# Kernel tuning notes

Measured on AMD Instinct MI355X. Metric: run time of the kernel, lower is better.

Reference implementation:

```python
import math
import jax, jax.numpy as jnp
import numpy as np

N, C, T, V = 256, 128, 64, 25
OUT, H = 128, 4
D = OUT // H  # 32
MAX_LEN = 64
KSIZE = 9
EPS = 1e-5
NEG = -1e9


def setup_inputs() -> dict:
    key = jax.random.key(0)
    ks = jax.random.split(key, 20)
    std = 0.02
    return {
        "x": jax.random.normal(ks[0], (N, C, T, V), jnp.float32),
        # BatchNorm (eval mode) on input
        "bn_gamma": 1.0 + 0.1 * jax.random.normal(ks[1], (C,), jnp.float32),
        "bn_beta": 0.1 * jax.random.normal(ks[2], (C,), jnp.float32),
        "bn_mean": 0.1 * jax.random.normal(ks[3], (C,), jnp.float32),
        "bn_var": jax.random.uniform(ks[4], (C,), jnp.float32, 0.5, 1.5),
        # 1x1 convs (qkv_kernel=1)
        "qk_w": std * jax.random.normal(ks[5], (2 * OUT, C), jnp.float32),
        "qk_b": std * jax.random.normal(ks[6], (2 * OUT,), jnp.float32),
        "v_w": std * jax.random.normal(ks[7], (OUT, C), jnp.float32),
        "v_b": std * jax.random.normal(ks[8], (OUT,), jnp.float32),
        "logit_scale": jnp.full((H, 1, 1), math.log(math.sqrt(D)), jnp.float32),
        "rel_pos_bias": std * jax.random.normal(ks[9], (H, 2 * MAX_LEN - 1), jnp.float32),
        "proj_w": std * jax.random.normal(ks[10], (OUT, OUT), jnp.float32),
        "proj_b": std * jax.random.normal(ks[11], (OUT,), jnp.float32),
        # output BatchNorm (eval mode)
        "bno_gamma": 1.0 + 0.1 * jax.random.normal(ks[12], (OUT,), jnp.float32),
        "bno_beta": 0.1 * jax.random.normal(ks[13], (OUT,), jnp.float32),
        "bno_mean": 0.1 * jax.random.normal(ks[14], (OUT,), jnp.float32),
        "bno_var": jax.random.uniform(ks[15], (OUT,), jnp.float32, 0.5, 1.5),
    }


def _bn(x, gamma, beta, mean, var):
    # eval-mode BatchNorm2d over channel dim of (N, C, T, V)
    inv = gamma / jnp.sqrt(var + EPS)
    return (x - mean[:, None, None]) * inv[:, None, None] + beta[:, None, None]


def reference(x, bn_gamma, bn_beta, bn_mean, bn_var, qk_w, qk_b, v_w, v_b,
              logit_scale, rel_pos_bias, proj_w, proj_b,
              bno_gamma, bno_beta, bno_mean, bno_var):
    n, c, t, v = x.shape
    x_in = x
    xb = _bn(x, bn_gamma, bn_beta, bn_mean, bn_var)

    # 1x1 conv qk: (n, 2*OUT, t, v) -> split into q, k of shape (n, v, h, t, d)
    qk = jnp.einsum('nctv,oc->notv', xb, qk_w) + qk_b[:, None, None]
    qk = qk.reshape(n, 2, H, D, t, v).transpose(1, 0, 5, 2, 4, 3)  # (2, n, v, h, t, d)
    q, k = qk[0], qk[1]
    val = (jnp.einsum('nctv,oc->notv', xb, v_w) + v_b[:, None, None])
    val = val.reshape(n, H, D, t, v).transpose(0, 4, 1, 3, 2)  # (n, v, h, t, d)

    # cosine-sim attention: L2-normalize q, k; learned per-head temperature
    scale = jnp.exp(jnp.minimum(logit_scale, math.log(100.0)))  # (h,1,1)
    q = q / jnp.maximum(jnp.linalg.norm(q, axis=-1, keepdims=True), 1e-12) * scale
    k = k / jnp.maximum(jnp.linalg.norm(k, axis=-1, keepdims=True), 1e-12)

    # SDPA applies an extra 1/sqrt(d) scale by default
    scores = jnp.einsum('nvhid,nvhjd->nvhij', q, k) / math.sqrt(D)

    coords = jnp.arange(t)
    rel_idx = coords[None, :] - coords[:, None] + (MAX_LEN - 1)  # (t, t)
    bias = rel_pos_bias[:, rel_idx]  # (h, t, t)
    local = jnp.abs(coords[:, None] - coords[None, :]) <= KSIZE // 2  # (t, t)

    scores = jnp.where(local[None, None, None], scores + bias[None, None], NEG)
    attn = jax.nn.softmax(scores, axis=-1)
    out = jnp.einsum('nvhij,nvhjd->nvhid', attn, val)  # (n, v, h, t, d)
    out = out.transpose(0, 2, 4, 3, 1).reshape(n, OUT, t, v)

    out = jnp.einsum('nctv,oc->notv', out, proj_w) + proj_b[:, None, None] + x_in
    # stride=1 -> pool is identity; ffn_ratio=0 -> no FFN; dropout=0
    out = _bn(out, bno_gamma, bno_beta, bno_mean, bno_var)
    return out
```

## Files before the change

kernel.cpp:

```cpp
#include <hip/hip_runtime.h>
#include <hip/hip_bf16.h>

typedef __attribute__((ext_vector_type(8))) short bf16x8;
typedef __attribute__((ext_vector_type(4))) float f32x4;

static __device__ __forceinline__ unsigned short f2bf(float f){
  __hip_bfloat16 h = __float2bfloat16(f);
  return __builtin_bit_cast(unsigned short, h);
}
static __device__ __forceinline__ unsigned int pk2(float a, float b){
  return (unsigned int)f2bf(a) | ((unsigned int)f2bf(b) << 16);
}
static __device__ __forceinline__ float bf2f(unsigned short h){
  return __uint_as_float(((unsigned int)h) << 16);
}
static __device__ __forceinline__ f32x4 mfma16(bf16x8 a, bf16x8 b, f32x4 c){
  return __builtin_amdgcn_mfma_f32_16x16x32_bf16(a, b, c, 0, 0, 0);
}

static __device__ __forceinline__ void prep_body(int g,
    const float* __restrict__ bn_g, const float* __restrict__ bn_b,
    const float* __restrict__ bn_m, const float* __restrict__ bn_v,
    const float* __restrict__ qk_w, const float* __restrict__ qk_b,
    const float* __restrict__ v_w,  const float* __restrict__ v_b,
    const float* __restrict__ ls,   const float* __restrict__ proj_w,
    const float* __restrict__ proj_b,
    const float* __restrict__ bo_g, const float* __restrict__ bo_b,
    const float* __restrict__ bo_m, const float* __restrict__ bo_v,
    unsigned short* __restrict__ Wqkv, unsigned short* __restrict__ Wp,
    float* __restrict__ bqf, float* __restrict__ bpf,
    float* __restrict__ rsf, float* __restrict__ shf)
{
  if (g < 384){
    const float* wr = (g < 256) ? (qk_w + g * 128) : (v_w + (g - 256) * 128);
    float acc = (g < 256) ? qk_b[g] : v_b[g - 256];
    for (int c = 0; c < 128; c++){
      float inv = bn_g[c] * rsqrtf(bn_v[c] + 1e-5f);
      float sh  = bn_b[c] - bn_m[c] * inv;
      float wv  = wr[c];
      Wqkv[g * 128 + c] = f2bf(wv * inv);
      acc += wv * sh;
    }
    bqf[g] = acc;
  } else if (g < 512){
    int o = g - 384;
    float invo = bo_g[o] * rsqrtf(bo_v[o] + 1e-5f);
    for (int c = 0; c < 128; c++)
      Wp[o * 128 + c] = f2bf(proj_w[o * 128 + c] * invo);
    bpf[o] = (proj_b[o] - bo_m[o]) * invo + bo_b[o];
    rsf[o] = invo;
    if (o < 4)
      shf[o] = expf(fminf(ls[o], 4.6051701859880914f)) * 0.17677669529663687f;
  }
}

__global__ void prep_kernel(
    const float* __restrict__ bn_g, const float* __restrict__ bn_b,
    const float* __restrict__ bn_m, const float* __restrict__ bn_v,
    const float* __restrict__ qk_w, const float* __restrict__ qk_b,
    const float* __restrict__ v_w,  const float* __restrict__ v_b,
    const float* __restrict__ ls,   const float* __restrict__ proj_w,
    const float* __restrict__ proj_b,
    const float* __restrict__ bo_g, const float* __restrict__ bo_b,
    const float* __restrict__ bo_m, const float* __restrict__ bo_v,
    unsigned short* __restrict__ Wqkv, unsigned short* __restrict__ Wp,
    float* __restrict__ bqf, float* __restrict__ bpf,
    float* __restrict__ rsf, float* __restrict__ shf)
{
  int g = blockIdx.x * 256 + threadIdx.x;
  prep_body(g, bn_g, bn_b, bn_m, bn_v, qk_w, qk_b, v_w, v_b, ls,
            proj_w, proj_b, bo_g, bo_b, bo_m, bo_v, Wqkv, Wp, bqf, bpf, rsf, shf);
}

__global__ __launch_bounds__(512) void pack_x(const float* __restrict__ x,
    unsigned short* __restrict__ xb,
    const float* __restrict__ bn_g, const float* __restrict__ bn_b,
    const float* __restrict__ bn_m, const float* __restrict__ bn_v,
    const float* __restrict__ qk_w, const float* __restrict__ qk_b,
    const float* __restrict__ v_w,  const float* __restrict__ v_b,
    const float* __restrict__ ls,   const float* __restrict__ proj_w,
    const float* __restrict__ proj_b,
    const float* __restrict__ bo_g, const float* __restrict__ bo_b,
    const float* __restrict__ bo_m, const float* __restrict__ bo_v,
    unsigned short* __restrict__ Wqkv, unsigned short* __restrict__ Wp,
    float* __restrict__ bqf, float* __restrict__ bpf,
    float* __restrict__ rsf, float* __restrict__ shf)
{
  __shared__ __align__(16) unsigned short tile[200][136];
  int n = blockIdx.x >> 3;
  int slab = blockIdx.x & 7;
  int t0 = slab * 8;
  int tid = threadIdx.x;
  const float* xn = x + (long)n * 204800 + (long)t0 * 25;
  for (int k = 0; k < 13; k++){
    int idx = tid + k * 512;
    if (idx < 6400){
      int c  = idx / 50;
      int r4 = idx - c * 50;
      float4 f = *((const float4*)(xn + (long)c * 1600 + r4 * 4));
      int sw = 8 * ((r4 >> 1) & 7);
      int cs = c ^ sw;
      tile[r4*4+0][cs] = f2bf(f.x);
      tile[r4*4+1][cs] = f2bf(f.y);
      tile[r4*4+2][cs] = f2bf(f.z);
      tile[r4*4+3][cs] = f2bf(f.w);
    }
  }
  __syncthreads();
  for (int k = 0; k < 7; k++){
    int idx = tid + k * 512;
    if (idx < 3200){
      int r  = idx >> 4;
      int u  = idx & 15;
      int lt = r / 25;
      int vv = r - lt * 25;
      int c0 = (u ^ lt) * 8;
      int sw = 8 * ((r >> 3) & 7);
      uint4 d = *((const uint4*)&tile[r][c0 ^ sw]);
      *((uint4*)(xb + ((long)(n * 25 + vv) * 64 + t0 + lt) * 128 + u * 8)) = d;
    }
  }
  if (blockIdx.x == 0)
    prep_body(tid, bn_g, bn_b, bn_m, bn_v, qk_w, qk_b, v_w, v_b, ls,
              proj_w, proj_b, bo_g, bo_b, bo_m, bo_v, Wqkv, Wp, bqf, bpf, rsf, shf);
}

__global__ __launch_bounds__(512) void unpack_out(const unsigned short* __restrict__ ob,
                                                  float* __restrict__ out)
{
  __shared__ __align__(16) unsigned short tile[200][136];
  int n = blockIdx.x >> 3;
  int slab = blockIdx.x & 7;
  int t0 = slab * 8;
  int tid = threadIdx.x;
  for (int k = 0; k < 7; k++){
    int idx = tid + k * 512;
    if (idx < 3200){
      int r  = idx >> 4;
      int u  = idx & 15;
      int lt = r / 25;
      int vv = r - lt * 25;
      uint4 d = *((const uint4*)(ob + ((long)(n * 25 + vv) * 64 + t0 + lt) * 128 + u * 8));
      int c0 = (u ^ lt) * 8;
      int sw = 8 * ((r >> 3) & 7);
      *((uint4*)&tile[r][c0 ^ sw]) = d;
    }
  }
  __syncthreads();
  float* on = out + (long)n * 204800 + (long)t0 * 25;
  for (int k = 0; k < 13; k++){
    int idx = tid + k * 512;
    if (idx < 6400){
      int c  = idx / 50;
      int r4 = idx - c * 50;
      int sw = 8 * ((r4 >> 1) & 7);
      int cs = c ^ sw;
      float4 f;
      f.x = bf2f(tile[r4*4+0][cs]);
      f.y = bf2f(tile[r4*4+1][cs]);
      f.z = bf2f(tile[r4*4+2][cs]);
      f.w = bf2f(tile[r4*4+3][cs]);
      *((float4*)(on + (long)c * 1600 + r4 * 4)) = f;
    }
  }
}

#define B_RA    0
#define B_RB    16384
#define B_BQ    49152
#define B_BP    50688
#define B_RS    51200
#define B_SH    51712
#define B_BIAS  51728
#define B_TOTAL 53760

__global__ __launch_bounds__(256, 3) void fused_compute(
    const unsigned short* __restrict__ xb,
    const unsigned short* __restrict__ Wqkv,
    const unsigned short* __restrict__ Wp,
    const float* __restrict__ bqf,
    const float* __restrict__ bpf,
    const float* __restrict__ rsf,
    const float* __restrict__ shf,
    const float* __restrict__ relb,
    unsigned short* __restrict__ ob)
{
  __shared__ __align__(16) char smem[B_TOTAL];
  char* ra = smem + B_RA;
  float* c_bq   = (float*)(smem + B_BQ);
  float* c_bp   = (float*)(smem + B_BP);
  float* c_rs   = (float*)(smem + B_RS);
  float* c_sh   = (float*)(smem + B_SH);
  float* c_bias = (float*)(smem + B_BIAS);

  int bid = blockIdx.x;
  int swz = (bid & 7) * 800 + (bid >> 3);
  long tileoff = (long)swz * 8192;
  int tid  = threadIdx.x;
  int lane = tid & 63;
  int w    = tid >> 6;
  int h    = w;
  int l4   = lane >> 4;
  int l15  = lane & 15;

  char* qkh = smem + B_RB + h * 8192;

  for (int i = tid; i < 384; i += 256) c_bq[i] = bqf[i];
  if (tid < 128){ c_bp[tid] = bpf[tid]; c_rs[tid] = rsf[tid]; }
  if (tid < 4) c_sh[tid] = shf[tid];
  for (int i = tid; i < 508; i += 256) c_bias[i] = relb[i];
  {
    const uint4* src = (const uint4*)(xb + tileoff);
    uint4* dst = (uint4*)ra;
    #pragma unroll
    for (int i = 0; i < 4; i++) dst[tid + i * 256] = src[tid + i * 256];
  }
  __syncthreads();

  const f32x4 zero4 = {0.f, 0.f, 0.f, 0.f};
  uint2 resid[2][4];

  {
    int rb[4] = {32*h, 32*h + 16, 128 + 32*h, 128 + 32*h + 16};
    f32x4 acc[4][4];
    #pragma unroll
    for (int m = 0; m < 4; m++)
      #pragma unroll
      for (int nt = 0; nt < 4; nt++) acc[m][nt] = zero4;
    #pragma unroll
    for (int ks = 0; ks < 4; ks++){
      int ko = ks * 32 + l4 * 8;
      bf16x8 a[4], b[4];
      #pragma unroll
      for (int m = 0; m < 4; m++)
        a[m] = *((const bf16x8*)(Wqkv + (rb[m] + l15) * 128 + ko));
      #pragma unroll
      for (int nt = 0; nt < 4; nt++){
        int row = nt * 16 + l15;
        b[nt] = *((const bf16x8*)(ra + row * 256 + ((ko * 2) ^ ((row & 7) << 4))));
      }
      #pragma unroll
      for (int m = 0; m < 4; m++)
        #pragma unroll
        for (int nt = 0; nt < 4; nt++)
          acc[m][nt] = mfma16(a[m], b[nt], acc[m][nt]);
    }
    #pragma unroll
    for (int m = 0; m < 4; m++)
      #pragma unroll
      for (int nt = 0; nt < 4; nt++)
        #pragma unroll
        for (int r = 0; r < 4; r++)
          acc[m][nt][r] += c_bq[rb[m] + l4 * 4 + r];

    #pragma unroll
    for (int nt = 0; nt < 4; nt++){
      float ssq = 0.f, ssk = 0.f;
      #pragma unroll
      for (int r = 0; r < 4; r++){
        ssq += acc[0][nt][r] * acc[0][nt][r] + acc[1][nt][r] * acc[1][nt][r];
        ssk += acc[2][nt][r] * acc[2][nt][r] + acc[3][nt][r] * acc[3][nt][r];
      }
      ssq += __shfl_xor(ssq, 16); ssq += __shfl_xor(ssq, 32);
      ssk += __shfl_xor(ssk, 16); ssk += __shfl_xor(ssk, 32);
      float scq = c_sh[h] / fmaxf(sqrtf(ssq), 1e-12f);
      float sck = 1.0f   / fmaxf(sqrtf(ssk), 1e-12f);
      int row = nt * 16 + l15;
      #pragma unroll
      for (int m = 0; m < 2; m++){
        uint2 p;
        p.x = pk2(acc[m][nt][0] * scq, acc[m][nt][1] * scq);
        p.y = pk2(acc[m][nt][2] * scq, acc[m][nt][3] * scq);
        *((uint2*)(qkh + row * 128 + ((m * 32 + l4 * 8) ^ ((row & 7) << 4)))) = p;
      }
      #pragma unroll
      for (int m = 2; m < 4; m++){
        uint2 p;
        p.x = pk2(acc[m][nt][0] * sck, acc[m][nt][1] * sck);
        p.y = pk2(acc[m][nt][2] * sck, acc[m][nt][3] * sck);
        *((uint2*)(qkh + row * 128 + ((64 + (m - 2) * 32 + l4 * 8) ^ ((row & 7) << 4)))) = p;
      }
    }
  }

  {
    int rb4 = 256 + 32 * h, rb5 = 256 + 32 * h + 16;
    f32x4 accv[2][4];
    #pragma unroll
    for (int m = 0; m < 2; m++)
      #pragma unroll
      for (int nt = 0; nt < 4; nt++) accv[m][nt] = zero4;
    #pragma unroll
    for (int ks = 0; ks < 4; ks++){
      int ko = ks * 32 + l4 * 8;
      bf16x8 a0 = *((const bf16x8*)(Wqkv + (rb4 + l15) * 128 + ko));
      bf16x8 a1 = *((const bf16x8*)(Wqkv + (rb5 + l15) * 128 + ko));
      #pragma unroll
      for (int nt = 0; nt < 4; nt++){
        int row = nt * 16 + l15;
        bf16x8 b = *((const bf16x8*)(ra + row * 256 + ((ko * 2) ^ ((row & 7) << 4))));
        accv[0][nt] = mfma16(a0, b, accv[0][nt]);
        accv[1][nt] = mfma16(a1, b, accv[1][nt]);
      }
    }
    #pragma unroll
    for (int mt = 0; mt < 2; mt++)
      #pragma unroll
      for (int nt = 0; nt < 4; nt++){
        int o0 = w * 32 + mt * 16 + l4 * 4;
        int t2 = nt * 16 + l15;
        resid[mt][nt] = *((const uint2*)(ra + t2 * 256 + ((o0 * 2) ^ ((t2 & 7) << 4))));
      }
    __syncthreads();

    #pragma unroll
    for (int m = 0; m < 2; m++)
      #pragma unroll
      for (int nt = 0; nt < 4; nt++)
        #pragma unroll
        for (int r = 0; r < 4; r++){
          int d = h * 32 + m * 16 + l4 * 4 + r;
          float vv = accv[m][nt][r] + c_bq[256 + h * 32 + m * 16 + l4 * 4 + r];
          *((unsigned short*)(ra + d * 128 + ((((nt * 16 + l15) * 2)) ^ ((d & 7) << 4)))) = f2bf(vv);
        }
  }
  __builtin_amdgcn_sched_barrier(0);

  bf16x8 kf[4], qf[4];
  {
    #pragma unroll
    for (int jt = 0; jt < 4; jt++){
      int row = jt * 16 + l15;
      kf[jt] = *((const bf16x8*)(qkh + row * 128 + ((64 + l4 * 16) ^ ((row & 7) << 4))));
    }
    #pragma unroll
    for (int it = 0; it < 4; it++){
      int row = it * 16 + l15;
      qf[it] = *((const bf16x8*)(qkh + row * 128 + ((l4 * 16) ^ ((row & 7) << 4))));
    }
  }
  __builtin_amdgcn_sched_barrier(0);

  {
    f32x4 sAcc[4][4];
    #pragma unroll
    for (int jt = 0; jt < 4; jt++)
      #pragma unroll
      for (int it = 0; it < 4; it++) sAcc[jt][it] = zero4;
    #pragma unroll
    for (int jt = 0; jt < 4; jt++)
      #pragma unroll
      for (int it = 0; it < 4; it++)
        if (jt <= it + 1 && it <= jt + 1)
          sAcc[jt][it] = mfma16(kf[jt], qf[it], sAcc[jt][it]);

    #pragma unroll
    for (int it = 0; it < 4; it++){
      int i = it * 16 + l15;
      float sv[16];
      float sum = 0.f;
      #pragma unroll
      for (int jt = 0; jt < 4; jt++){
        if (jt + 1 < it || jt > it + 1) continue;
        #pragma unroll
        for (int r = 0; r < 4; r++){
          int j = jt * 16 + l4 * 4 + r;
          int rel = j - i;
          float s = sAcc[jt][it][r] + c_bias[h * 127 + rel + 63];
          bool inb = (rel >= -4) && (rel <= 4);
          float p = inb ? __expf(s) : 0.f;
          sv[jt * 4 + r] = p;
          sum += p;
        }
      }
      sum += __shfl_xor(sum, 16);
      sum += __shfl_xor(sum, 32);
      float rs = 1.0f / sum;
      #pragma unroll
      for (int jt = 0; jt < 4; jt++){
        uint2 p;
        if (jt + 1 < it || jt > it + 1){
          p.x = 0u; p.y = 0u;
        } else {
          p.x = pk2(sv[jt*4+0] * rs, sv[jt*4+1] * rs);
          p.y = pk2(sv[jt*4+2] * rs, sv[jt*4+3] * rs);
        }
        *((uint2*)(qkh + i * 128 + ((jt * 32 + l4 * 8) ^ ((i & 7) << 4)))) = p;
      }
    }
  }
  __builtin_amdgcn_sched_barrier(0);

  bf16x8 av[2][2], bv2[4][2];
  {
    #pragma unroll
    for (int mt = 0; mt < 2; mt++)
      #pragma unroll
      for (int ks2 = 0; ks2 < 2; ks2++){
        int row = h * 32 + mt * 16 + l15;
        av[mt][ks2] = *((const bf16x8*)(ra + row * 128 + ((ks2 * 64 + l4 * 16) ^ ((row & 7) << 4))));
      }
    #pragma unroll
    for (int it = 0; it < 4; it++)
      #pragma unroll
      for (int ks2 = 0; ks2 < 2; ks2++){
        int row = it * 16 + l15;
        bv2[it][ks2] = *((const bf16x8*)(qkh + row * 128 + ((ks2 * 64 + l4 * 16) ^ ((row & 7) << 4))));
      }
  }
  __syncthreads();

  unsigned short* ao = (unsigned short*)(smem + B_RB);
  {
    f32x4 pAcc[2][4];
    #pragma unroll
    for (int mt = 0; mt < 2; mt++)
      #pragma unroll
      for (int it = 0; it < 4; it++) pAcc[mt][it] = zero4;
    #pragma unroll
    for (int mt = 0; mt < 2; mt++)
      #pragma unroll
      for (int it = 0; it < 4; it++)
        #pragma unroll
        for (int ks2 = 0; ks2 < 2; ks2++)
          pAcc[mt][it] = mfma16(av[mt][ks2], bv2[it][ks2], pAcc[mt][it]);
    #pragma unroll
    for (int mt = 0; mt < 2; mt++)
      #pragma unroll
      for (int it = 0; it < 4; it++){
        int d0 = mt * 16 + l4 * 4;
        int i  = it * 16 + l15;
        uint2 p;
        p.x = pk2(pAcc[mt][it][0], pAcc[mt][it][1]);
        p.y = pk2(pAcc[mt][it][2], pAcc[mt][it][3]);
        *((uint2*)&ao[i * 136 + h * 32 + d0]) = p;
      }
  }
  __syncthreads();

  {
    f32x4 acc2[2][4];
    #pragma unroll
    for (int mt = 0; mt < 2; mt++)
      #pragma unroll
      for (int nt = 0; nt < 4; nt++) acc2[mt][nt] = zero4;
    #pragma unroll
    for (int ks = 0; ks < 4; ks++){
      int ko = ks * 32 + l4 * 8;
      bf16x8 a2[2], b2[4];
      #pragma unroll
      for (int mt = 0; mt < 2; mt++)
        a2[mt] = *((const bf16x8*)(Wp + (w * 32 + mt * 16 + l15) * 128 + ko));
      #pragma unroll
      for (int nt = 0; nt < 4; nt++)
        b2[nt] = *((const bf16x8*)&ao[(nt * 16 + l15) * 136 + ko]);
      #pragma unroll
      for (int mt = 0; mt < 2; mt++)
        #pragma unroll
        for (int nt = 0; nt < 4; nt++)
          acc2[mt][nt] = mfma16(a2[mt], b2[nt], acc2[mt][nt]);
    }
    #pragma unroll
    for (int mt = 0; mt < 2; mt++)
      #pragma unroll
      for (int nt = 0; nt < 4; nt++){
        int o0 = w * 32 + mt * 16 + l4 * 4;
        int t2 = nt * 16 + l15;
        uint2 rd = resid[mt][nt];
        float r0 = bf2f((unsigned short)(rd.x & 0xFFFFu));
        float r1f = bf2f((unsigned short)(rd.x >> 16));
        float r2 = bf2f((unsigned short)(rd.y & 0xFFFFu));
        float r3 = bf2f((unsigned short)(rd.y >> 16));
        uint2 p;
        p.x = pk2(acc2[mt][nt][0] + c_bp[o0+0] + r0 * c_rs[o0+0],
                  acc2[mt][nt][1] + c_bp[o0+1] + r1f * c_rs[o0+1]);
        p.y = pk2(acc2[mt][nt][2] + c_bp[o0+2] + r2 * c_rs[o0+2],
                  acc2[mt][nt][3] + c_bp[o0+3] + r3 * c_rs[o0+3]);
        *((uint2*)(ra + t2 * 256 + ((o0 * 2) ^ ((t2 & 7) << 4)))) = p;
      }
  }
  __syncthreads();
  {
    const uint4* sxl = (const uint4*)ra;
    uint4* obt = (uint4*)(ob + tileoff);
    #pragma unroll
    for (int i = 0; i < 4; i++) obt[tid + i * 256] = sxl[tid + i * 256];
  }
}

#define F_X     0
#define F_RB    17408
#define F_VT    58368
#define F_BQ    76800
#define F_BP    78336
#define F_RS    78848
#define F_SH    79360
#define F_BIAS  79376
#define F_TOTAL 81408

__global__ __launch_bounds__(256, 2) void fused_scatter(
    const float* __restrict__ x,
    const unsigned short* __restrict__ Wqkv,
    const unsigned short* __restrict__ Wp,
    const float* __restrict__ bqf,
    const float* __restrict__ bpf,
    const float* __restrict__ rsf,
    const float* __restrict__ shf,
    const float* __restrict__ relb,
    float* __restrict__ out)
{
  __shared__ __align__(16) char smem[F_TOTAL];
  unsigned short* xl   = (unsigned short*)(smem + F_X);
  unsigned short* rbu  = (unsigned short*)(smem + F_RB);
  unsigned short* vT   = (unsigned short*)(smem + F_VT);
  float* c_bq   = (float*)(smem + F_BQ);
  float* c_bp   = (float*)(smem + F_BP);
  float* c_rs   = (float*)(smem + F_RS);
  float* c_sh   = (float*)(smem + F_SH);
  float* c_bias = (float*)(smem + F_BIAS);

  int bid = blockIdx.x;
  int swz = (bid & 7) * 800 + (bid >> 3);
  int n = swz / 25;
  int v = swz - n * 25;
  int tid  = threadIdx.x;
  int lane = tid & 63;
  int w    = tid >> 6;
  int l4   = lane >> 4;
  int l15  = lane & 15;

  for (int i = tid; i < 384; i += 256) c_bq[i] = bqf[i];
  if (tid < 128){ c_bp[tid] = bpf[tid]; c_rs[tid] = rsf[tid]; }
  if (tid < 4) c_sh[tid] = shf[tid];
  for (int i = tid; i < 508; i += 256) c_bias[i] = relb[i];

  {
    const float* xb2 = x + (long)n * 204800 + v;
    int t  = lane;
    int cg = w * 32;
    #pragma unroll
    for (int i = 0; i < 4; i++){
      unsigned int pk[4];
      #pragma unroll
      for (int e = 0; e < 4; e++){
        int c = cg + i * 8 + e * 2;
        pk[e] = pk2(xb2[(long)c * 1600 + t * 25], xb2[(long)(c + 1) * 1600 + t * 25]);
      }
      uint4 q4; q4.x = pk[0]; q4.y = pk[1]; q4.z = pk[2]; q4.w = pk[3];
      *((uint4*)&xl[t * 136 + cg + i * 8]) = q4;
    }
  }
  __syncthreads();

  const f32x4 zero4 = {0.f, 0.f, 0.f, 0.f};

  {
    f32x4 acc[6][4];
    #pragma unroll
    for (int m = 0; m < 6; m++)
      #pragma unroll
      for (int nt = 0; nt < 4; nt++) acc[m][nt] = zero4;
    int Mb = w * 96;
    #pragma unroll
    for (int ks = 0; ks < 4; ks++){
      int ko = ks * 32 + l4 * 8;
      bf16x8 a[6], b[4];
      #pragma unroll
      for (int m = 0; m < 6; m++)
        a[m] = *((const bf16x8*)(Wqkv + (Mb + m * 16 + l15) * 128 + ko));
      #pragma unroll
      for (int nt = 0; nt < 4; nt++)
        b[nt] = *((const bf16x8*)&xl[(nt * 16 + l15) * 136 + ko]);
      #pragma unroll
      for (int m = 0; m < 6; m++)
        #pragma unroll
        for (int nt = 0; nt < 4; nt++)
          acc[m][nt] = mfma16(a[m], b[nt], acc[m][nt]);
    }
    #pragma unroll
    for (int m = 0; m < 6; m++){
      #pragma unroll
      for (int nt = 0; nt < 4; nt++){
        #pragma unroll
        for (int r = 0; r < 4; r++){
          int o  = Mb + m * 16 + l4 * 4 + r;
          int t2 = nt * 16 + l15;
          unsigned short bv = f2bf(acc[m][nt][r] + c_bq[o]);
          if (o < 256){
            rbu[(((o >> 7) * 4 + ((o >> 5) & 3)) * 64 + t2) * 40 + (o & 31)] = bv;
          } else {
            vT[(o - 256) * 72 + t2] = bv;
          }
        }
      }
    }
  }
  __syncthreads();

  {
    #pragma unroll
    for (int rr = 0; rr < 2; rr++){
      int r = tid + rr * 256;
      unsigned short* row = &rbu[r * 40];
      uint4 u0 = *((uint4*)(row + 0));
      uint4 u1 = *((uint4*)(row + 8));
      uint4 u2 = *((uint4*)(row + 16));
      uint4 u3 = *((uint4*)(row + 24));
      unsigned int uu[16] = {u0.x,u0.y,u0.z,u0.w, u1.x,u1.y,u1.z,u1.w,
                             u2.x,u2.y,u2.z,u2.w, u3.x,u3.y,u3.z,u3.w};
      float vals[32];
      float ss = 0.f;
      #pragma unroll
      for (int k2 = 0; k2 < 16; k2++){
        float f0 = bf2f((unsigned short)(uu[k2] & 0xFFFFu));
        float f1 = bf2f((unsigned short)(uu[k2] >> 16));
        vals[2*k2] = f0; vals[2*k2+1] = f1;
        ss += f0 * f0 + f1 * f1;
      }
      float sc = 1.0f / fmaxf(sqrtf(ss), 1e-12f);
      if (r < 256) sc *= c_sh[(r >> 6) & 3];
      #pragma unroll
      for (int k2 = 0; k2 < 16; k2++)
        uu[k2] = pk2(vals[2*k2] * sc, vals[2*k2+1] * sc);
      u0.x=uu[0];u0.y=uu[1];u0.z=uu[2];u0.w=uu[3];
      u1.x=uu[4];u1.y=uu[5];u1.z=uu[6];u1.w=uu[7];
      u2.x=uu[8];u2.y=uu[9];u2.z=uu[10];u2.w=uu[11];
      u3.x=uu[12];u3.y=uu[13];u3.z=uu[14];u3.w=uu[15];
      *((uint4*)(row + 0))  = u0;
      *((uint4*)(row + 8))  = u1;
      *((uint4*)(row + 16)) = u2;
      *((uint4*)(row + 24)) = u3;
    }
  }
  __syncthreads();

  int h = w;
  bf16x8 kf[4], qf[4];
  {
    const unsigned short* kb = &rbu[(256 + h * 64) * 40];
    const unsigned short* qb = &rbu[(h * 64) * 40];
    int ko = l4 * 8;
    #pragma unroll
    for (int jt = 0; jt < 4; jt++)
      kf[jt] = *((const bf16x8*)(kb + (jt * 16 + l15) * 40 + ko));
    #pragma unroll
    for (int it = 0; it < 4; it++)
      qf[it] = *((const bf16x8*)(qb + (it * 16 + l15) * 40 + ko));
  }
  __syncthreads();

  unsigned short* attn = rbu + h * 4608;
  {
    f32x4 sAcc[4][4];
    #pragma unroll
    for (int jt = 0; jt < 4; jt++)
      #pragma unroll
      for (int it = 0; it < 4; it++) sAcc[jt][it] = zero4;
    #pragma unroll
    for (int jt = 0; jt < 4; jt++)
      #pragma unroll
      for (int it = 0; it < 4; it++)
        sAcc[jt][it] = mfma16(kf[jt], qf[it], sAcc[jt][it]);

    #pragma unroll
    for (int it = 0; it < 4; it++){
      int i = it * 16 + l15;
      float sv[16];
      float mx = -1e30f;
      #pragma unroll
      for (int jt = 0; jt < 4; jt++){
        #pragma unroll
        for (int r = 0; r < 4; r++){
          int j = jt * 16 + l4 * 4 + r;
          int rel = j - i;
          float s;
          if (rel < -4 || rel > 4) s = -1e9f;
          else s = sAcc[jt][it][r] + c_bias[h * 127 + rel + 63];
          sv[jt * 4 + r] = s;
          mx = fmaxf(mx, s);
        }
      }
      mx = fmaxf(mx, __shfl_xor(mx, 16));
      mx = fmaxf(mx, __shfl_xor(mx, 32));
      float sum = 0.f;
      #pragma unroll
      for (int k2 = 0; k2 < 16; k2++){
        float p = __expf(sv[k2] - mx);
        sv[k2] = p; sum += p;
      }
      sum += __shfl_xor(sum, 16);
      sum += __shfl_xor(sum, 32);
      float rs = 1.0f / sum;
      #pragma unroll
      for (int jt = 0; jt < 4; jt++)
        #pragma unroll
        for (int r = 0; r < 4; r++)
          attn[i * 72 + (jt * 16 + l4 * 4 + r)] = f2bf(sv[jt * 4 + r] * rs);
    }
  }

  bf16x8 av[2][2], bv2[4][2];
  {
    int ko = l4 * 8;
    #pragma unroll
    for (int mt = 0; mt < 2; mt++)
      #pragma unroll
      for (int ks2 = 0; ks2 < 2; ks2++)
        av[mt][ks2] = *((const bf16x8*)&vT[(h * 32 + mt * 16 + l15) * 72 + ks2 * 32 + ko]);
    #pragma unroll
    for (int it = 0; it < 4; it++)
      #pragma unroll
      for (int ks2 = 0; ks2 < 2; ks2++)
        bv2[it][ks2] = *((const bf16x8*)&attn[(it * 16 + l15) * 72 + ks2 * 32 + ko]);
  }
  __syncthreads();

  unsigned short* ao = rbu;
  {
    f32x4 pAcc[2][4];
    #pragma unroll
    for (int mt = 0; mt < 2; mt++)
      #pragma unroll
      for (int it = 0; it < 4; it++) pAcc[mt][it] = zero4;
    #pragma unroll
    for (int mt = 0; mt < 2; mt++)
      #pragma unroll
      for (int it = 0; it < 4; it++)
        #pragma unroll
        for (int ks2 = 0; ks2 < 2; ks2++)
          pAcc[mt][it] = mfma16(av[mt][ks2], bv2[it][ks2], pAcc[mt][it]);
    #pragma unroll
    for (int mt = 0; mt < 2; mt++)
      #pragma unroll
      for (int it = 0; it < 4; it++)
        #pragma unroll
        for (int r = 0; r < 4; r++){
          int d = mt * 16 + l4 * 4 + r;
          int i = it * 16 + l15;
          ao[i * 136 + h * 32 + d] = f2bf(pAcc[mt][it][r]);
        }
  }
  __syncthreads();

  {
    f32x4 acc2[2][4];
    #pragma unroll
    for (int mt = 0; mt < 2; mt++)
      #pragma unroll
      for (int nt = 0; nt < 4; nt++) acc2[mt][nt] = zero4;
    #pragma unroll
    for (int ks = 0; ks < 4; ks++){
      int ko = ks * 32 + l4 * 8;
      bf16x8 a2[2], b2[4];
      #pragma unroll
      for (int mt = 0; mt < 2; mt++)
        a2[mt] = *((const bf16x8*)(Wp + (w * 32 + mt * 16 + l15) * 128 + ko));
      #pragma unroll
      for (int nt = 0; nt < 4; nt++)
        b2[nt] = *((const bf16x8*)&ao[(nt * 16 + l15) * 136 + ko]);
      #pragma unroll
      for (int mt = 0; mt < 2; mt++)
        #pragma unroll
        for (int nt = 0; nt < 4; nt++)
          acc2[mt][nt] = mfma16(a2[mt], b2[nt], acc2[mt][nt]);
    }
    float* outp = out + (long)n * 204800 + v;
    #pragma unroll
    for (int mt = 0; mt < 2; mt++)
      #pragma unroll
      for (int nt = 0; nt < 4; nt++)
        #pragma unroll
        for (int r = 0; r < 4; r++){
          int o  = w * 32 + mt * 16 + l4 * 4 + r;
          int t2 = nt * 16 + l15;
          float val = acc2[mt][nt][r] + c_bp[o] + bf2f(xl[t2 * 136 + o]) * c_rs[o];
          outp[(long)o * 1600 + t2 * 25] = val;
        }
  }
}

extern "C" void kernel_launch(void* const* d_in, const int* in_sizes, int n_in,
                              void* d_out, int out_size, void* d_ws, size_t ws_size,
                              hipStream_t stream)
{
  const float* x     = (const float*)d_in[0];
  const float* bn_g  = (const float*)d_in[1];
  const float* bn_b  = (const float*)d_in[2];
  const float* bn_m  = (const float*)d_in[3];
  const float* bn_v  = (const float*)d_in[4];
  const float* qk_w  = (const float*)d_in[5];
  const float* qk_b  = (const float*)d_in[6];
  const float* v_w   = (const float*)d_in[7];
  const float* v_b   = (const float*)d_in[8];
  const float* ls    = (const float*)d_in[9];
  const float* relb  = (const float*)d_in[10];
  const float* pj_w  = (const float*)d_in[11];
  const float* pj_b  = (const float*)d_in[12];
  const float* bo_g  = (const float*)d_in[13];
  const float* bo_b  = (const float*)d_in[14];
  const float* bo_m  = (const float*)d_in[15];
  const float* bo_v  = (const float*)d_in[16];

  const size_t XB_BYTES = 104857600;
  const size_t NEED = 2 * XB_BYTES + 98304 + 32768 + 1536 + 512 + 512 + 16;

  char* ws = (char*)d_ws;
  size_t wbase = (ws_size >= NEED) ? (2 * XB_BYTES) : 0;

  unsigned short* Wqkv = (unsigned short*)(ws + wbase);
  unsigned short* Wp   = (unsigned short*)(ws + wbase + 98304);
  float* bqf = (float*)(ws + wbase + 131072);
  float* bpf = (float*)(ws + wbase + 132608);
  float* rsf = (float*)(ws + wbase + 133120);
  float* shf = (float*)(ws + wbase + 133632);

  if (ws_size >= NEED){
    unsigned short* xb = (unsigned short*)(ws);
    unsigned short* ob = (unsigned short*)(ws + XB_BYTES);
    hipLaunchKernelGGL(pack_x, dim3(2048), dim3(512), 0, stream, x, xb,
                       bn_g, bn_b, bn_m, bn_v, qk_w, qk_b, v_w, v_b, ls,
                       pj_w, pj_b, bo_g, bo_b, bo_m, bo_v,
                       Wqkv, Wp, bqf, bpf, rsf, shf);
    hipLaunchKernelGGL(fused_compute, dim3(6400), dim3(256), 0, stream,
                       xb, Wqkv, Wp, bqf, bpf, rsf, shf, relb, ob);
    hipLaunchKernelGGL(unpack_out, dim3(2048), dim3(512), 0, stream, ob, (float*)d_out);
  } else {
    hipLaunchKernelGGL(prep_kernel, dim3(2), dim3(256), 0, stream,
                       bn_g, bn_b, bn_m, bn_v, qk_w, qk_b, v_w, v_b, ls,
                       pj_w, pj_b, bo_g, bo_b, bo_m, bo_v,
                       Wqkv, Wp, bqf, bpf, rsf, shf);
    hipLaunchKernelGGL(fused_scatter, dim3(6400), dim3(256), 0, stream,
                       x, Wqkv, Wp, bqf, bpf, rsf, shf, relb, (float*)d_out);
  }
}
```

Measured before the change: 299.6 us.

## Fuse input transpose into compute kernel via strided gather, drop pack_x

Removes the pack_x kernel that transposed x into a bf16 workspace. The compute kernel now gathers its (n,v) column straight from the fp32 input with strided loads, converts to bf16 and writes a swizzled LDS tile. Weight prep moves back to a separate small prep kernel. This saves a full write and re-read of the intermediate buffer, but each gather load is strided by 25 floats, so coalescing is poor and the same cache lines are fetched by up to 25 different blocks.

```diff
diff --git a/kernel.cpp b/kernel.cpp
--- a/kernel.cpp
+++ b/kernel.cpp
@@ -16,42 +16,6 @@
 }
 static __device__ __forceinline__ f32x4 mfma16(bf16x8 a, bf16x8 b, f32x4 c){
   return __builtin_amdgcn_mfma_f32_16x16x32_bf16(a, b, c, 0, 0, 0);
-}
-
-static __device__ __forceinline__ void prep_body(int g,
-    const float* __restrict__ bn_g, const float* __restrict__ bn_b,
-    const float* __restrict__ bn_m, const float* __restrict__ bn_v,
-    const float* __restrict__ qk_w, const float* __restrict__ qk_b,
-    const float* __restrict__ v_w,  const float* __restrict__ v_b,
-    const float* __restrict__ ls,   const float* __restrict__ proj_w,
-    const float* __restrict__ proj_b,
-    const float* __restrict__ bo_g, const float* __restrict__ bo_b,
-    const float* __restrict__ bo_m, const float* __restrict__ bo_v,
-    unsigned short* __restrict__ Wqkv, unsigned short* __restrict__ Wp,
-    float* __restrict__ bqf, float* __restrict__ bpf,
-    float* __restrict__ rsf, float* __restrict__ shf)
-{
-  if (g < 384){
-    const float* wr = (g < 256) ? (qk_w + g * 128) : (v_w + (g - 256) * 128);
-    float acc = (g < 256) ? qk_b[g] : v_b[g - 256];
-    for (int c = 0; c < 128; c++){
-      float inv = bn_g[c] * rsqrtf(bn_v[c] + 1e-5f);
-      float sh  = bn_b[c] - bn_m[c] * inv;
-      float wv  = wr[c];
-      Wqkv[g * 128 + c] = f2bf(wv * inv);
-      acc += wv * sh;
-    }
-    bqf[g] = acc;
-  } else if (g < 512){
-    int o = g - 384;
-    float invo = bo_g[o] * rsqrtf(bo_v[o] + 1e-5f);
-    for (int c = 0; c < 128; c++)
-      Wp[o * 128 + c] = f2bf(proj_w[o * 128 + c] * invo);
-    bpf[o] = (proj_b[o] - bo_m[o]) * invo + bo_b[o];
-    rsf[o] = invo;
-    if (o < 4)
-      shf[o] = expf(fminf(ls[o], 4.6051701859880914f)) * 0.17677669529663687f;
-  }
 }
 
 __global__ void prep_kernel(
@@ -68,61 +32,27 @@
     float* __restrict__ rsf, float* __restrict__ shf)
 {
   int g = blockIdx.x * 256 + threadIdx.x;
-  prep_body(g, bn_g, bn_b, bn_m, bn_v, qk_w, qk_b, v_w, v_b, ls,
-            proj_w, proj_b, bo_g, bo_b, bo_m, bo_v, Wqkv, Wp, bqf, bpf, rsf, shf);
-}
-
-__global__ __launch_bounds__(512) void pack_x(const float* __restrict__ x,
-    unsigned short* __restrict__ xb,
-    const float* __restrict__ bn_g, const float* __restrict__ bn_b,
-    const float* __restrict__ bn_m, const float* __restrict__ bn_v,
-    const float* __restrict__ qk_w, const float* __restrict__ qk_b,
-    const float* __restrict__ v_w,  const float* __restrict__ v_b,
-    const float* __restrict__ ls,   const float* __restrict__ proj_w,
-    const float* __restrict__ proj_b,
-    const float* __restrict__ bo_g, const float* __restrict__ bo_b,
-    const float* __restrict__ bo_m, const float* __restrict__ bo_v,
-    unsigned short* __restrict__ Wqkv, unsigned short* __restrict__ Wp,
-    float* __restrict__ bqf, float* __restrict__ bpf,
-    float* __restrict__ rsf, float* __restrict__ shf)
-{
-  __shared__ __align__(16) unsigned short tile[200][136];
-  int n = blockIdx.x >> 3;
-  int slab = blockIdx.x & 7;
-  int t0 = slab * 8;
-  int tid = threadIdx.x;
-  const float* xn = x + (long)n * 204800 + (long)t0 * 25;
-  for (int k = 0; k < 13; k++){
-    int idx = tid + k * 512;
-    if (idx < 6400){
-      int c  = idx / 50;
-      int r4 = idx - c * 50;
-      float4 f = *((const float4*)(xn + (long)c * 1600 + r4 * 4));
-      int sw = 8 * ((r4 >> 1) & 7);
-      int cs = c ^ sw;
-      tile[r4*4+0][cs] = f2bf(f.x);
-      tile[r4*4+1][cs] = f2bf(f.y);
-      tile[r4*4+2][cs] = f2bf(f.z);
-      tile[r4*4+3][cs] = f2bf(f.w);
-    }
-  }
-  __syncthreads();
-  for (int k = 0; k < 7; k++){
-    int idx = tid + k * 512;
-    if (idx < 3200){
-      int r  = idx >> 4;
-      int u  = idx & 15;
-      int lt = r / 25;
-      int vv = r - lt * 25;
-      int c0 = (u ^ lt) * 8;
-      int sw = 8 * ((r >> 3) & 7);
-      uint4 d = *((const uint4*)&tile[r][c0 ^ sw]);
-      *((uint4*)(xb + ((long)(n * 25 + vv) * 64 + t0 + lt) * 128 + u * 8)) = d;
-    }
-  }
-  if (blockIdx.x == 0)
-    prep_body(tid, bn_g, bn_b, bn_m, bn_v, qk_w, qk_b, v_w, v_b, ls,
-              proj_w, proj_b, bo_g, bo_b, bo_m, bo_v, Wqkv, Wp, bqf, bpf, rsf, shf);
+  if (g < 384){
+    const float* wr = (g < 256) ? (qk_w + g * 128) : (v_w + (g - 256) * 128);
+    float acc = (g < 256) ? qk_b[g] : v_b[g - 256];
+    for (int c = 0; c < 128; c++){
+      float inv = bn_g[c] * rsqrtf(bn_v[c] + 1e-5f);
+      float sh  = bn_b[c] - bn_m[c] * inv;
+      float wv  = wr[c];
+      Wqkv[g * 128 + c] = f2bf(wv * inv);
+      acc += wv * sh;
+    }
+    bqf[g] = acc;
+  } else if (g < 512){
+    int o = g - 384;
+    float invo = bo_g[o] * rsqrtf(bo_v[o] + 1e-5f);
+    for (int c = 0; c < 128; c++)
+      Wp[o * 128 + c] = f2bf(proj_w[o * 128 + c] * invo);
+    bpf[o] = (proj_b[o] - bo_m[o]) * invo + bo_b[o];
+    rsf[o] = invo;
+    if (o < 4)
+      shf[o] = expf(fminf(ls[o], 4.6051701859880914f)) * 0.17677669529663687f;
+  }
 }
 
 __global__ __launch_bounds__(512) void unpack_out(const unsigned short* __restrict__ ob,
@@ -174,8 +104,8 @@
 #define B_BIAS  51728
 #define B_TOTAL 53760
 
-__global__ __launch_bounds__(256, 3) void fused_compute(
-    const unsigned short* __restrict__ xb,
+__global__ __launch_bounds__(256, 3) void fused_gather(
+    const float* __restrict__ x,
     const unsigned short* __restrict__ Wqkv,
     const unsigned short* __restrict__ Wp,
     const float* __restrict__ bqf,
@@ -195,6 +125,8 @@
 
   int bid = blockIdx.x;
   int swz = (bid & 7) * 800 + (bid >> 3);
+  int n = swz / 25;
+  int v = swz - n * 25;
   long tileoff = (long)swz * 8192;
   int tid  = threadIdx.x;
   int lane = tid & 63;
@@ -205,15 +137,31 @@
 
   char* qkh = smem + B_RB + h * 8192;
 
+  const float* xn = x + (long)n * 204800 + v;
+  float xv[32];
+  {
+    int t = lane;
+    #pragma unroll
+    for (int i = 0; i < 4; i++)
+      #pragma unroll
+      for (int e = 0; e < 8; e++)
+        xv[i * 8 + e] = xn[(long)(w * 32 + i * 8 + e) * 1600 + t * 25];
+  }
   for (int i = tid; i < 384; i += 256) c_bq[i] = bqf[i];
   if (tid < 128){ c_bp[tid] = bpf[tid]; c_rs[tid] = rsf[tid]; }
   if (tid < 4) c_sh[tid] = shf[tid];
   for (int i = tid; i < 508; i += 256) c_bias[i] = relb[i];
   {
-    const uint4* src = (const uint4*)(xb + tileoff);
-    uint4* dst = (uint4*)ra;
-    #pragma unroll
-    for (int i = 0; i < 4; i++) dst[tid + i * 256] = src[tid + i * 256];
+    int t = lane;
+    #pragma unroll
+    for (int i = 0; i < 4; i++){
+      uint4 q4;
+      q4.x = pk2(xv[i*8+0], xv[i*8+1]);
+      q4.y = pk2(xv[i*8+2], xv[i*8+3]);
+      q4.z = pk2(xv[i*8+4], xv[i*8+5]);
+      q4.w = pk2(xv[i*8+6], xv[i*8+7]);
+      *((uint4*)(ra + t * 256 + (((w * 4 + i) ^ (t & 7)) << 4))) = q4;
+    }
   }
   __syncthreads();
 
@@ -802,10 +750,10 @@
   const float* bo_v  = (const float*)d_in[16];
 
   const size_t XB_BYTES = 104857600;
-  const size_t NEED = 2 * XB_BYTES + 98304 + 32768 + 1536 + 512 + 512 + 16;
+  const size_t NEED = XB_BYTES + 98304 + 32768 + 1536 + 512 + 512 + 16;
 
   char* ws = (char*)d_ws;
-  size_t wbase = (ws_size >= NEED) ? (2 * XB_BYTES) : 0;
+  size_t wbase = (ws_size >= NEED) ? XB_BYTES : 0;
 
   unsigned short* Wqkv = (unsigned short*)(ws + wbase);
   unsigned short* Wp   = (unsigned short*)(ws + wbase + 98304);
@@ -814,21 +762,17 @@
   float* rsf = (float*)(ws + wbase + 133120);
   float* shf = (float*)(ws + wbase + 133632);
 
+  hipLaunchKernelGGL(prep_kernel, dim3(2), dim3(256), 0, stream,
+                     bn_g, bn_b, bn_m, bn_v, qk_w, qk_b, v_w, v_b, ls,
+                     pj_w, pj_b, bo_g, bo_b, bo_m, bo_v,
+                     Wqkv, Wp, bqf, bpf, rsf, shf);
+
   if (ws_size >= NEED){
-    unsigned short* xb = (unsigned short*)(ws);
-    unsigned short* ob = (unsigned short*)(ws + XB_BYTES);
-    hipLaunchKernelGGL(pack_x, dim3(2048), dim3(512), 0, stream, x, xb,
-                       bn_g, bn_b, bn_m, bn_v, qk_w, qk_b, v_w, v_b, ls,
-                       pj_w, pj_b, bo_g, bo_b, bo_m, bo_v,
-                       Wqkv, Wp, bqf, bpf, rsf, shf);
-    hipLaunchKernelGGL(fused_compute, dim3(6400), dim3(256), 0, stream,
-                       xb, Wqkv, Wp, bqf, bpf, rsf, shf, relb, ob);
+    unsigned short* ob = (unsigned short*)(ws);
+    hipLaunchKernelGGL(fused_gather, dim3(6400), dim3(256), 0, stream,
+                       x, Wqkv, Wp, bqf, bpf, rsf, shf, relb, ob);
     hipLaunchKernelGGL(unpack_out, dim3(2048), dim3(512), 0, stream, ob, (float*)d_out);
   } else {
-    hipLaunchKernelGGL(prep_kernel, dim3(2), dim3(256), 0, stream,
-                       bn_g, bn_b, bn_m, bn_v, qk_w, qk_b, v_w, v_b, ls,
-                       pj_w, pj_b, bo_g, bo_b, bo_m, bo_v,
-                       Wqkv, Wp, bqf, bpf, rsf, shf);
     hipLaunchKernelGGL(fused_scatter, dim3(6400), dim3(256), 0, stream,
                        x, Wqkv, Wp, bqf, bpf, rsf, shf, relb, (float*)d_out);
   }
```

Measured after the change: 367.3 us. 22.6% more time.
